# Performance work log

Measured on AMD Instinct MI355X. Metric: run time of the kernel, lower is better.

Reference implementation:

```python
import jax, jax.numpy as jnp
import numpy as np

DIM = 1024
NUM_EXPERTS = 8
TOP_K = 2
HIDDEN = int(DIM * 1.5)  # 1536, matches expert_dim = int(dim * 1.5)


def setup_inputs() -> dict:
    key = jax.random.key(0)
    k_x, k_r, k_w1, k_w2, k_w3 = jax.random.split(key, 5)
    B, T = 2, 4096
    s_in = 1.0 / np.sqrt(DIM)
    s_h = 1.0 / np.sqrt(HIDDEN)
    return {
        "x": jax.random.normal(k_x, (B, T, DIM), dtype=jnp.float32),
        # router: Linear(dim, num_experts, bias=False) -> stored as [C, E]
        "Wr": jax.random.uniform(k_r, (DIM, NUM_EXPERTS), minval=-s_in, maxval=s_in, dtype=jnp.float32),
        # stacked expert weights: w1/w3 [E, C, H], w2 [E, H, C]
        "W1": jax.random.uniform(k_w1, (NUM_EXPERTS, DIM, HIDDEN), minval=-s_in, maxval=s_in, dtype=jnp.float32),
        "W2": jax.random.uniform(k_w2, (NUM_EXPERTS, HIDDEN, DIM), minval=-s_h, maxval=s_h, dtype=jnp.float32),
        "W3": jax.random.uniform(k_w3, (NUM_EXPERTS, DIM, HIDDEN), minval=-s_in, maxval=s_in, dtype=jnp.float32),
    }


def reference(x, Wr, W1, W2, W3):
    B, T, C = x.shape
    xf = x.reshape(-1, C)  # [N, C]
    gate_logits = xf @ Wr  # [N, E]
    w, idx = jax.lax.top_k(gate_logits, TOP_K)  # [N, K]
    w = jax.nn.softmax(w, axis=-1)
    # dense combine weights: zero for non-selected experts -> [N, E]
    comb = jnp.sum(w[:, :, None] * jax.nn.one_hot(idx, NUM_EXPERTS, dtype=w.dtype), axis=1)
    # SwiGLU for all experts (masked-out experts contribute with weight 0)
    h = jnp.einsum('nc,ech->neh', xf, W1)  # [N, E, H]
    g = jnp.einsum('nc,ech->neh', xf, W3)  # [N, E, H]
    y = jnp.einsum('neh,ehc->nec', jax.nn.silu(h) * g, W2)  # [N, E, C]
    out = jnp.einsum('nec,ne->nc', y, comb)
    return out.reshape(B, T, C)
```

## Files before the change

### kernel.cpp

```cpp
#include <hip/hip_runtime.h>
#include <hip/hip_bf16.h>
#include <math.h>

#define DIM   1024
#define NEXP  8
#define HID   1536
#define NTOK  8192
#define NPOS  16384
#define PADR  128

typedef __attribute__((ext_vector_type(8))) short bf16x8;
typedef __attribute__((ext_vector_type(4))) float floatx4;

__device__ __forceinline__ unsigned short f2bf(float f) {
  unsigned int u = __float_as_uint(f);
  u += 0x7FFFu + ((u >> 16) & 1u);
  return (unsigned short)(u >> 16);
}

__device__ __forceinline__ float bf2f(unsigned short h) {
  return __uint_as_float((unsigned int)h << 16);
}

__device__ __forceinline__ void async_cp16(void* lds, const void* g) {
  __builtin_amdgcn_global_load_lds(
      (const __attribute__((address_space(1))) unsigned int*)g,
      (__attribute__((address_space(3))) unsigned int*)lds, 16, 0, 0);
}

__device__ __forceinline__ int2 cnt_off(const int* __restrict__ hdr, int e) {
  int s = 0, c = 0;
#pragma unroll
  for (int i = 0; i < NEXP; ++i) {
    const int v = hdr[i];
    if (i < e) s += v;
    if (i == e) c = v;
  }
  return make_int2(c, s);
}

__global__ __launch_bounds__(256) void moe_router(
    const float* __restrict__ x, const float* __restrict__ Wr,
    int* __restrict__ meta_e, float* __restrict__ meta_w) {
  const int wave = threadIdx.x >> 6, lane = threadIdx.x & 63;
  const int token = blockIdx.x * 4 + wave;
  const float* xr = x + (size_t)token * DIM;
  float acc[NEXP];
#pragma unroll
  for (int e = 0; e < NEXP; ++e) acc[e] = 0.f;
  for (int i = lane; i < DIM; i += 64) {
    const float xv = xr[i];
    const float* wr = Wr + (size_t)i * NEXP;
#pragma unroll
    for (int e = 0; e < NEXP; ++e) acc[e] += xv * wr[e];
  }
#pragma unroll
  for (int off = 32; off > 0; off >>= 1) {
#pragma unroll
    for (int e = 0; e < NEXP; ++e) acc[e] += __shfl_down(acc[e], off);
  }
  if (lane == 0) {
    int i0 = 0; float v0 = acc[0];
#pragma unroll
    for (int e = 1; e < NEXP; ++e) if (acc[e] > v0) { v0 = acc[e]; i0 = e; }
    int i1 = -1; float v1 = -3.4e38f;
#pragma unroll
    for (int e = 0; e < NEXP; ++e) if (e != i0 && acc[e] > v1) { v1 = acc[e]; i1 = e; }
    const float w0 = 1.f / (1.f + expf(v1 - v0));
    meta_e[token * 2 + 0] = i0;
    meta_e[token * 2 + 1] = i1;
    meta_w[token * 2 + 0] = w0;
    meta_w[token * 2 + 1] = 1.f - w0;
  }
}

__global__ __launch_bounds__(256) void moe_hist(
    const int* __restrict__ meta_e, int* __restrict__ hdr) {
  const int idx = blockIdx.x * 256 + threadIdx.x;
  const int lane = threadIdx.x & 63;
  const int e = meta_e[idx];
#pragma unroll
  for (int ex = 0; ex < NEXP; ++ex) {
    const unsigned long long m = __ballot(e == ex);
    if (m && lane == 0) atomicAdd(&hdr[ex], __popcll(m));
  }
}

__global__ __launch_bounds__(256) void moe_build(
    const int* __restrict__ meta_e, int* __restrict__ hdr,
    int* __restrict__ tok, int* __restrict__ inv) {
  const int idx = blockIdx.x * 256 + threadIdx.x;
  const int lane = threadIdx.x & 63;
  const int token = idx >> 1;
  const int e = meta_e[idx];
  int pos = 0;
#pragma unroll
  for (int ex = 0; ex < NEXP; ++ex) {
    const unsigned long long m = __ballot(e == ex);
    if (m) {
      const int leader = (int)__ffsll((long long)m) - 1;
      int base = 0;
      if (lane == leader) base = atomicAdd(&hdr[16 + ex], __popcll(m));
      base = __shfl(base, leader);
      if (e == ex) {
        const int2 co = cnt_off(hdr, ex);
        pos = co.y + base + (int)__popcll(m & ((1ull << lane) - 1ull));
      }
    }
  }
  tok[pos] = token;
  inv[idx] = pos;
}

__global__ __launch_bounds__(256) void moe_gather(
    const float* __restrict__ x, const int* __restrict__ tok,
    unsigned short* __restrict__ Xg) {
  const int pos = blockIdx.x;
  const int t = tok[pos];
  const float4 v = ((const float4*)(x + (size_t)t * DIM))[threadIdx.x];
  ushort4 o = make_ushort4(f2bf(v.x), f2bf(v.y), f2bf(v.z), f2bf(v.w));
  ((ushort4*)(Xg + (size_t)pos * DIM))[threadIdx.x] = o;
}

__global__ __launch_bounds__(256) void moe_transpose_all(
    const float* __restrict__ W1, const float* __restrict__ W3,
    const float* __restrict__ W2,
    unsigned short* __restrict__ W1t, unsigned short* __restrict__ W3t,
    unsigned short* __restrict__ W2t) {
  __shared__ float tile[64][65];
  const int z = blockIdx.z;
  const int which = z >> 3, e = z & 7;
  const float* src; unsigned short* dst; int R, C;
  if (which == 0)      { src = W1; dst = W1t; R = DIM; C = HID; }
  else if (which == 1) { src = W3; dst = W3t; R = DIM; C = HID; }
  else                 { src = W2; dst = W2t; R = HID; C = DIM; }
  const int nbx = C / 64;
  const int bx = blockIdx.x % nbx, by = blockIdx.x / nbx;
  const float* ein = src + (size_t)e * R * C;
  unsigned short* eout = dst + (size_t)e * R * C;
  const int c0 = bx * 64, r0 = by * 64;
  const int lx = threadIdx.x & 15, ly = threadIdx.x >> 4;
#pragma unroll
  for (int it = 0; it < 4; ++it) {
    const int r = ly + it * 16;
    const float4 v = *(const float4*)&ein[(size_t)(r0 + r) * C + c0 + lx * 4];
    tile[r][lx * 4 + 0] = v.x;
    tile[r][lx * 4 + 1] = v.y;
    tile[r][lx * 4 + 2] = v.z;
    tile[r][lx * 4 + 3] = v.w;
  }
  __syncthreads();
#pragma unroll
  for (int it = 0; it < 4; ++it) {
    const int cc = ly + it * 16;
    ushort4 o = make_ushort4(f2bf(tile[lx * 4 + 0][cc]), f2bf(tile[lx * 4 + 1][cc]),
                             f2bf(tile[lx * 4 + 2][cc]), f2bf(tile[lx * 4 + 3][cc]));
    *(ushort4*)&eout[(size_t)(c0 + cc) * R + r0 + lx * 4] = o;
  }
}


__global__ __launch_bounds__(256) void moe_gemm1(
    const unsigned short* __restrict__ Xg,
    const unsigned short* __restrict__ W1t,
    const unsigned short* __restrict__ W3t,
    unsigned short* __restrict__ Hbuf,
    const int* __restrict__ hdr) {
  const int e = blockIdx.y;
  const int NT = HID / 64;
  const int tileRow = blockIdx.x / NT;
  const int tileN = blockIdx.x % NT;
  const int2 co = cnt_off(hdr, e);
  const int cnt = co.x;
  if (tileRow * 128 >= cnt) return;
  const int off = co.y;
  const size_t tileM = (size_t)off + (size_t)tileRow * 128;
  const int n0 = tileN * 64;

  __shared__ unsigned short As[2][128 * 32];
  __shared__ unsigned short B1s[2][64 * 32];
  __shared__ unsigned short B3s[2][64 * 32];

  const int lane = threadIdx.x & 63;
  const int wave = threadIdx.x >> 6;
  const int wm = wave >> 1, wn = wave & 1;
  const int rsub = lane >> 2;
  const int ksw  = (((lane & 3) ^ ((lane >> 3) & 3))) * 8;
  const int kf   = (((lane >> 4) ^ ((lane >> 1) & 3))) * 8;

  const unsigned short* Abase = Xg + tileM * DIM;
  const unsigned short* B1base = W1t + ((size_t)e * HID + n0) * DIM;
  const unsigned short* B3base = W3t + ((size_t)e * HID + n0) * DIM;

  floatx4 zero = {0.f, 0.f, 0.f, 0.f};
  floatx4 acc_h[4][2], acc_g[4][2];
#pragma unroll
  for (int i = 0; i < 4; ++i)
#pragma unroll
    for (int j = 0; j < 2; ++j) { acc_h[i][j] = zero; acc_g[i][j] = zero; }

  for (int k0 = 0; k0 < DIM; k0 += 64) {
#pragma unroll
    for (int h = 0; h < 2; ++h) {
      const int kk = k0 + h * 32;
#pragma unroll
      for (int t = 0; t < 2; ++t) {
        const int c = wave * 2 + t;
        const int row = c * 16 + rsub;
        async_cp16(&As[h][c * 512], Abase + (size_t)row * DIM + kk + ksw);
      }
      const int row = wave * 16 + rsub;
      async_cp16(&B1s[h][wave * 512], B1base + (size_t)row * DIM + kk + ksw);
      async_cp16(&B3s[h][wave * 512], B3base + (size_t)row * DIM + kk + ksw);
    }
    __syncthreads();
#pragma unroll
    for (int h = 0; h < 2; ++h) {
      bf16x8 a[4], b1[2], b3[2];
#pragma unroll
      for (int i = 0; i < 4; ++i)
        a[i] = *(const bf16x8*)&As[h][(wm * 64 + i * 16 + (lane & 15)) * 32 + kf];
#pragma unroll
      for (int j = 0; j < 2; ++j) {
        b1[j] = *(const bf16x8*)&B1s[h][(wn * 32 + j * 16 + (lane & 15)) * 32 + kf];
        b3[j] = *(const bf16x8*)&B3s[h][(wn * 32 + j * 16 + (lane & 15)) * 32 + kf];
      }
#pragma unroll
      for (int i = 0; i < 4; ++i)
#pragma unroll
        for (int j = 0; j < 2; ++j) {
          acc_h[i][j] = __builtin_amdgcn_mfma_f32_16x16x32_bf16(a[i], b1[j], acc_h[i][j], 0, 0, 0);
          acc_g[i][j] = __builtin_amdgcn_mfma_f32_16x16x32_bf16(a[i], b3[j], acc_g[i][j], 0, 0, 0);
        }
    }
    __syncthreads();
  }

  const int r0 = (lane >> 4) * 4;
  const int cc = lane & 15;
#pragma unroll
  for (int i = 0; i < 4; ++i)
#pragma unroll
    for (int r = 0; r < 4; ++r) {
      const int lrow = tileRow * 128 + wm * 64 + i * 16 + r0 + r;
      if (lrow < cnt) {
        unsigned short* hrow = Hbuf + (size_t)(off + lrow) * HID + n0 + wn * 32 + cc;
#pragma unroll
        for (int j = 0; j < 2; ++j) {
          const float h = acc_h[i][j][r];
          const float g = acc_g[i][j][r];
          const float s = h / (1.f + expf(-h));
          hrow[j * 16] = f2bf(s * g);
        }
      }
    }
}

__global__ __launch_bounds__(256) void moe_gemm2(
    const unsigned short* __restrict__ Hbuf,
    const unsigned short* __restrict__ W2t,
    const int* __restrict__ hdr,
    unsigned short* __restrict__ Y) {
  const int e = blockIdx.y;
  const int NT = DIM / 128;
  const int tileRow = blockIdx.x / NT;
  const int tileN = blockIdx.x % NT;
  const int2 co = cnt_off(hdr, e);
  const int cnt = co.x;
  if (tileRow * 128 >= cnt) return;
  const int off = co.y;
  const size_t tileM = (size_t)off + (size_t)tileRow * 128;
  const int n0 = tileN * 128;

  __shared__ unsigned short As[2][128 * 32];
  __shared__ unsigned short Bs[2][128 * 32];

  const int lane = threadIdx.x & 63;
  const int wave = threadIdx.x >> 6;
  const int wm = wave >> 1, wn = wave & 1;
  const int rsub = lane >> 2;
  const int ksw  = (((lane & 3) ^ ((lane >> 3) & 3))) * 8;
  const int kf   = (((lane >> 4) ^ ((lane >> 1) & 3))) * 8;

  const unsigned short* Abase = Hbuf + tileM * HID;
  const unsigned short* Bbase = W2t + ((size_t)e * DIM + n0) * HID;

  floatx4 zero = {0.f, 0.f, 0.f, 0.f};
  floatx4 acc[4][4];
#pragma unroll
  for (int i = 0; i < 4; ++i)
#pragma unroll
    for (int j = 0; j < 4; ++j) acc[i][j] = zero;

  for (int k0 = 0; k0 < HID; k0 += 64) {
#pragma unroll
    for (int h = 0; h < 2; ++h) {
      const int kk = k0 + h * 32;
#pragma unroll
      for (int t = 0; t < 2; ++t) {
        const int c = wave * 2 + t;
        const int row = c * 16 + rsub;
        async_cp16(&As[h][c * 512], Abase + (size_t)row * HID + kk + ksw);
      }
#pragma unroll
      for (int t = 0; t < 2; ++t) {
        const int c = wave * 2 + t;
        const int row = c * 16 + rsub;
        async_cp16(&Bs[h][c * 512], Bbase + (size_t)row * HID + kk + ksw);
      }
    }
    __syncthreads();
#pragma unroll
    for (int h = 0; h < 2; ++h) {
      bf16x8 a[4], b[4];
#pragma unroll
      for (int i = 0; i < 4; ++i)
        a[i] = *(const bf16x8*)&As[h][(wm * 64 + i * 16 + (lane & 15)) * 32 + kf];
#pragma unroll
      for (int j = 0; j < 4; ++j)
        b[j] = *(const bf16x8*)&Bs[h][(wn * 64 + j * 16 + (lane & 15)) * 32 + kf];
#pragma unroll
      for (int i = 0; i < 4; ++i)
#pragma unroll
        for (int j = 0; j < 4; ++j)
          acc[i][j] = __builtin_amdgcn_mfma_f32_16x16x32_bf16(a[i], b[j], acc[i][j], 0, 0, 0);
    }
    __syncthreads();
  }

  const int r0 = (lane >> 4) * 4;
  const int cc = lane & 15;
#pragma unroll
  for (int i = 0; i < 4; ++i)
#pragma unroll
    for (int r = 0; r < 4; ++r) {
      const int lrow = tileRow * 128 + wm * 64 + i * 16 + r0 + r;
      if (lrow < cnt) {
        unsigned short* yrow = Y + (size_t)(off + lrow) * DIM + n0 + wn * 64 + cc;
#pragma unroll
        for (int j = 0; j < 4; ++j)
          yrow[j * 16] = f2bf(acc[i][j][r]);
      }
    }
}

__global__ __launch_bounds__(256) void moe_combine(
    const unsigned short* __restrict__ Y, const int* __restrict__ inv,
    const float* __restrict__ meta_w, float* __restrict__ out) {
  const int t = blockIdx.x;
  const int p0 = inv[t * 2 + 0], p1 = inv[t * 2 + 1];
  const float w0 = meta_w[t * 2 + 0], w1 = meta_w[t * 2 + 1];
  const ushort4 a = ((const ushort4*)(Y + (size_t)p0 * DIM))[threadIdx.x];
  const ushort4 b = ((const ushort4*)(Y + (size_t)p1 * DIM))[threadIdx.x];
  float4 o;
  o.x = w0 * bf2f(a.x) + w1 * bf2f(b.x);
  o.y = w0 * bf2f(a.y) + w1 * bf2f(b.y);
  o.z = w0 * bf2f(a.z) + w1 * bf2f(b.z);
  o.w = w0 * bf2f(a.w) + w1 * bf2f(b.w);
  ((float4*)(out + (size_t)t * DIM))[threadIdx.x] = o;
}

extern "C" void kernel_launch(void* const* d_in, const int* in_sizes, int n_in,
                              void* d_out, int out_size, void* d_ws, size_t ws_size,
                              hipStream_t stream) {
  const float* x  = (const float*)d_in[0];
  const float* Wr = (const float*)d_in[1];
  const float* W1 = (const float*)d_in[2];
  const float* W2 = (const float*)d_in[3];
  const float* W3 = (const float*)d_in[4];
  float* out = (float*)d_out;

  char* p = (char*)d_ws;
  auto carve = [&](size_t bytes) { char* r = p; p += (bytes + 255) & ~(size_t)255; return r; };

  int*            hdr    = (int*)carve(256);
  int*            meta_e = (int*)carve((size_t)NTOK * 2 * sizeof(int));
  float*          meta_w = (float*)carve((size_t)NTOK * 2 * sizeof(float));
  int*            tok    = (int*)carve((size_t)NPOS * sizeof(int));
  int*            inv    = (int*)carve((size_t)NTOK * 2 * sizeof(int));
  unsigned short* Xg     = (unsigned short*)carve((size_t)(NPOS + PADR) * DIM * 2);
  unsigned short* Hbuf   = (unsigned short*)carve((size_t)(NPOS + PADR) * HID * 2);
  unsigned short* W1t    = (unsigned short*)carve((size_t)NEXP * HID * DIM * 2);
  unsigned short* W3t    = (unsigned short*)carve((size_t)NEXP * HID * DIM * 2);
  unsigned short* W2t    = (unsigned short*)carve((size_t)NEXP * DIM * HID * 2);
  unsigned short* Y      = Xg;

  hipMemsetAsync(hdr, 0, 256, stream);

  moe_router<<<NTOK / 4, 256, 0, stream>>>(x, Wr, meta_e, meta_w);
  moe_hist<<<NPOS / 256, 256, 0, stream>>>(meta_e, hdr);
  moe_build<<<NPOS / 256, 256, 0, stream>>>(meta_e, hdr, tok, inv);
  moe_gather<<<NPOS, 256, 0, stream>>>(x, tok, Xg);

  moe_transpose_all<<<dim3(384, 1, 24), dim3(256), 0, stream>>>(W1, W3, W2, W1t, W3t, W2t);

  moe_gemm1<<<dim3(64 * (HID / 64), NEXP), 256, 0, stream>>>(Xg, W1t, W3t, Hbuf, hdr);
  moe_gemm2<<<dim3(64 * (DIM / 128), NEXP), 256, 0, stream>>>(Hbuf, W2t, hdr, Y);
  moe_combine<<<NTOK, 256, 0, stream>>>(Y, inv, meta_w, out);
}
```

Before: 525.8 us.

## Double-buffer MoE GEMM K-loop, persistent tile-row loop, wider transpose stores

Both expert GEMMs now issue async copies for the next 32-wide K slice into the alternate LDS buffer while computing on the current one, replacing the load-all-then-compute pattern with one sync per slice. The grid is shrunk so each block loops over tile rows with stride 16 instead of launching 64 row slots and exiting early, which cuts idle block launches. The weight transpose now writes 16-byte packed bf16 stores instead of 8-byte ones. The risk is less parallelism per expert when token counts are unbalanced, and extra LDS reads in the transpose may cause bank conflicts.

```diff
diff --git a/kernel.cpp b/kernel.cpp
--- a/kernel.cpp
+++ b/kernel.cpp
@@ -150,12 +150,17 @@
     tile[r][lx * 4 + 3] = v.w;
   }
   __syncthreads();
-#pragma unroll
-  for (int it = 0; it < 4; ++it) {
-    const int cc = ly + it * 16;
-    ushort4 o = make_ushort4(f2bf(tile[lx * 4 + 0][cc]), f2bf(tile[lx * 4 + 1][cc]),
-                             f2bf(tile[lx * 4 + 2][cc]), f2bf(tile[lx * 4 + 3][cc]));
-    *(ushort4*)&eout[(size_t)(c0 + cc) * R + r0 + lx * 4] = o;
+  const int r8 = (threadIdx.x & 7) * 8;
+  const int ccb = threadIdx.x >> 3;
+#pragma unroll
+  for (int it = 0; it < 2; ++it) {
+    const int cc = ccb + it * 32;
+    unsigned int w0 = (unsigned int)f2bf(tile[r8 + 0][cc]) | ((unsigned int)f2bf(tile[r8 + 1][cc]) << 16);
+    unsigned int w1 = (unsigned int)f2bf(tile[r8 + 2][cc]) | ((unsigned int)f2bf(tile[r8 + 3][cc]) << 16);
+    unsigned int w2 = (unsigned int)f2bf(tile[r8 + 4][cc]) | ((unsigned int)f2bf(tile[r8 + 5][cc]) << 16);
+    unsigned int w3 = (unsigned int)f2bf(tile[r8 + 6][cc]) | ((unsigned int)f2bf(tile[r8 + 7][cc]) << 16);
+    uint4 o = make_uint4(w0, w1, w2, w3);
+    *(uint4*)&eout[(size_t)(c0 + cc) * R + r0 + r8] = o;
   }
 }
 
@@ -168,13 +173,12 @@
     const int* __restrict__ hdr) {
   const int e = blockIdx.y;
   const int NT = HID / 64;
-  const int tileRow = blockIdx.x / NT;
+  const int TROW = 16;
   const int tileN = blockIdx.x % NT;
+  const int tr0 = blockIdx.x / NT;
   const int2 co = cnt_off(hdr, e);
   const int cnt = co.x;
-  if (tileRow * 128 >= cnt) return;
   const int off = co.y;
-  const size_t tileM = (size_t)off + (size_t)tileRow * 128;
   const int n0 = tileN * 64;
 
   __shared__ unsigned short As[2][128 * 32];
@@ -188,72 +192,77 @@
   const int ksw  = (((lane & 3) ^ ((lane >> 3) & 3))) * 8;
   const int kf   = (((lane >> 4) ^ ((lane >> 1) & 3))) * 8;
 
-  const unsigned short* Abase = Xg + tileM * DIM;
   const unsigned short* B1base = W1t + ((size_t)e * HID + n0) * DIM;
   const unsigned short* B3base = W3t + ((size_t)e * HID + n0) * DIM;
+  const unsigned short* Abase;
 
   floatx4 zero = {0.f, 0.f, 0.f, 0.f};
   floatx4 acc_h[4][2], acc_g[4][2];
-#pragma unroll
-  for (int i = 0; i < 4; ++i)
-#pragma unroll
-    for (int j = 0; j < 2; ++j) { acc_h[i][j] = zero; acc_g[i][j] = zero; }
-
-  for (int k0 = 0; k0 < DIM; k0 += 64) {
-#pragma unroll
-    for (int h = 0; h < 2; ++h) {
-      const int kk = k0 + h * 32;
-#pragma unroll
-      for (int t = 0; t < 2; ++t) {
-        const int c = wave * 2 + t;
-        const int row = c * 16 + rsub;
-        async_cp16(&As[h][c * 512], Abase + (size_t)row * DIM + kk + ksw);
+
+  auto stage = [&](int b, int kk) {
+#pragma unroll
+    for (int t2 = 0; t2 < 2; ++t2) {
+      const int c = wave * 2 + t2;
+      async_cp16(&As[b][c * 512], Abase + (size_t)(c * 16 + rsub) * DIM + kk + ksw);
+    }
+    async_cp16(&B1s[b][wave * 512], B1base + (size_t)(wave * 16 + rsub) * DIM + kk + ksw);
+    async_cp16(&B3s[b][wave * 512], B3base + (size_t)(wave * 16 + rsub) * DIM + kk + ksw);
+  };
+  auto compute = [&](int b) {
+    bf16x8 a[4], b1[2], b3[2];
+#pragma unroll
+    for (int i = 0; i < 4; ++i)
+      a[i] = *(const bf16x8*)&As[b][(wm * 64 + i * 16 + (lane & 15)) * 32 + kf];
+#pragma unroll
+    for (int j = 0; j < 2; ++j) {
+      b1[j] = *(const bf16x8*)&B1s[b][(wn * 32 + j * 16 + (lane & 15)) * 32 + kf];
+      b3[j] = *(const bf16x8*)&B3s[b][(wn * 32 + j * 16 + (lane & 15)) * 32 + kf];
+    }
+#pragma unroll
+    for (int i = 0; i < 4; ++i)
+#pragma unroll
+      for (int j = 0; j < 2; ++j) {
+        acc_h[i][j] = __builtin_amdgcn_mfma_f32_16x16x32_bf16(a[i], b1[j], acc_h[i][j], 0, 0, 0);
+        acc_g[i][j] = __builtin_amdgcn_mfma_f32_16x16x32_bf16(a[i], b3[j], acc_g[i][j], 0, 0, 0);
       }
-      const int row = wave * 16 + rsub;
-      async_cp16(&B1s[h][wave * 512], B1base + (size_t)row * DIM + kk + ksw);
-      async_cp16(&B3s[h][wave * 512], B3base + (size_t)row * DIM + kk + ksw);
-    }
+  };
+
+  for (int tileRow = tr0; tileRow * 128 < cnt; tileRow += TROW) {
+    Abase = Xg + ((size_t)off + (size_t)tileRow * 128) * DIM;
+#pragma unroll
+    for (int i = 0; i < 4; ++i)
+#pragma unroll
+      for (int j = 0; j < 2; ++j) { acc_h[i][j] = zero; acc_g[i][j] = zero; }
+
+    stage(0, 0);
     __syncthreads();
-#pragma unroll
-    for (int h = 0; h < 2; ++h) {
-      bf16x8 a[4], b1[2], b3[2];
-#pragma unroll
-      for (int i = 0; i < 4; ++i)
-        a[i] = *(const bf16x8*)&As[h][(wm * 64 + i * 16 + (lane & 15)) * 32 + kf];
-#pragma unroll
-      for (int j = 0; j < 2; ++j) {
-        b1[j] = *(const bf16x8*)&B1s[h][(wn * 32 + j * 16 + (lane & 15)) * 32 + kf];
-        b3[j] = *(const bf16x8*)&B3s[h][(wn * 32 + j * 16 + (lane & 15)) * 32 + kf];
-      }
-#pragma unroll
-      for (int i = 0; i < 4; ++i)
-#pragma unroll
-        for (int j = 0; j < 2; ++j) {
-          acc_h[i][j] = __builtin_amdgcn_mfma_f32_16x16x32_bf16(a[i], b1[j], acc_h[i][j], 0, 0, 0);
-          acc_g[i][j] = __builtin_amdgcn_mfma_f32_16x16x32_bf16(a[i], b3[j], acc_g[i][j], 0, 0, 0);
-        }
-    }
-    __syncthreads();
-  }
-
-  const int r0 = (lane >> 4) * 4;
-  const int cc = lane & 15;
-#pragma unroll
-  for (int i = 0; i < 4; ++i)
-#pragma unroll
-    for (int r = 0; r < 4; ++r) {
-      const int lrow = tileRow * 128 + wm * 64 + i * 16 + r0 + r;
-      if (lrow < cnt) {
-        unsigned short* hrow = Hbuf + (size_t)(off + lrow) * HID + n0 + wn * 32 + cc;
-#pragma unroll
-        for (int j = 0; j < 2; ++j) {
-          const float h = acc_h[i][j][r];
-          const float g = acc_g[i][j][r];
-          const float s = h / (1.f + expf(-h));
-          hrow[j * 16] = f2bf(s * g);
+#pragma unroll 1
+    for (int kt = 0; kt < 15; ++kt) {
+      stage(1, (2 * kt + 1) * 32); compute(0); __syncthreads();
+      stage(0, (2 * kt + 2) * 32); compute(1); __syncthreads();
+    }
+    stage(1, 31 * 32); compute(0); __syncthreads();
+    compute(1);
+
+    const int r0 = (lane >> 4) * 4;
+    const int cc = lane & 15;
+#pragma unroll
+    for (int i = 0; i < 4; ++i)
+#pragma unroll
+      for (int r = 0; r < 4; ++r) {
+        const int lrow = tileRow * 128 + wm * 64 + i * 16 + r0 + r;
+        if (lrow < cnt) {
+          unsigned short* hrow = Hbuf + (size_t)(off + lrow) * HID + n0 + wn * 32 + cc;
+#pragma unroll
+          for (int j = 0; j < 2; ++j) {
+            const float h = acc_h[i][j][r];
+            const float g = acc_g[i][j][r];
+            const float s = h / (1.f + expf(-h));
+            hrow[j * 16] = f2bf(s * g);
+          }
         }
       }
-    }
+  }
 }
 
 __global__ __launch_bounds__(256) void moe_gemm2(
@@ -263,13 +272,12 @@
     unsigned short* __restrict__ Y) {
   const int e = blockIdx.y;
   const int NT = DIM / 128;
-  const int tileRow = blockIdx.x / NT;
+  const int TROW = 16;
   const int tileN = blockIdx.x % NT;
+  const int tr0 = blockIdx.x / NT;
   const int2 co = cnt_off(hdr, e);
   const int cnt = co.x;
-  if (tileRow * 128 >= cnt) return;
   const int off = co.y;
-  const size_t tileM = (size_t)off + (size_t)tileRow * 128;
   const int n0 = tileN * 128;
 
   __shared__ unsigned short As[2][128 * 32];
@@ -282,66 +290,67 @@
   const int ksw  = (((lane & 3) ^ ((lane >> 3) & 3))) * 8;
   const int kf   = (((lane >> 4) ^ ((lane >> 1) & 3))) * 8;
 
-  const unsigned short* Abase = Hbuf + tileM * HID;
   const unsigned short* Bbase = W2t + ((size_t)e * DIM + n0) * HID;
+  const unsigned short* Abase;
 
   floatx4 zero = {0.f, 0.f, 0.f, 0.f};
   floatx4 acc[4][4];
-#pragma unroll
-  for (int i = 0; i < 4; ++i)
-#pragma unroll
-    for (int j = 0; j < 4; ++j) acc[i][j] = zero;
-
-  for (int k0 = 0; k0 < HID; k0 += 64) {
-#pragma unroll
-    for (int h = 0; h < 2; ++h) {
-      const int kk = k0 + h * 32;
-#pragma unroll
-      for (int t = 0; t < 2; ++t) {
-        const int c = wave * 2 + t;
-        const int row = c * 16 + rsub;
-        async_cp16(&As[h][c * 512], Abase + (size_t)row * HID + kk + ksw);
+
+  auto stage = [&](int b, int kk) {
+#pragma unroll
+    for (int t2 = 0; t2 < 2; ++t2) {
+      const int c = wave * 2 + t2;
+      async_cp16(&As[b][c * 512], Abase + (size_t)(c * 16 + rsub) * HID + kk + ksw);
+      async_cp16(&Bs[b][c * 512], Bbase + (size_t)(c * 16 + rsub) * HID + kk + ksw);
+    }
+  };
+  auto compute = [&](int bb) {
+    bf16x8 a[4], b[4];
+#pragma unroll
+    for (int i = 0; i < 4; ++i)
+      a[i] = *(const bf16x8*)&As[bb][(wm * 64 + i * 16 + (lane & 15)) * 32 + kf];
+#pragma unroll
+    for (int j = 0; j < 4; ++j)
+      b[j] = *(const bf16x8*)&Bs[bb][(wn * 64 + j * 16 + (lane & 15)) * 32 + kf];
+#pragma unroll
+    for (int i = 0; i < 4; ++i)
+#pragma unroll
+      for (int j = 0; j < 4; ++j)
+        acc[i][j] = __builtin_amdgcn_mfma_f32_16x16x32_bf16(a[i], b[j], acc[i][j], 0, 0, 0);
+  };
+
+  for (int tileRow = tr0; tileRow * 128 < cnt; tileRow += TROW) {
+    Abase = Hbuf + ((size_t)off + (size_t)tileRow * 128) * HID;
+#pragma unroll
+    for (int i = 0; i < 4; ++i)
+#pragma unroll
+      for (int j = 0; j < 4; ++j) acc[i][j] = zero;
+
+    stage(0, 0);
+    __syncthreads();
+#pragma unroll 1
+    for (int kt = 0; kt < 23; ++kt) {
+      stage(1, (2 * kt + 1) * 32); compute(0); __syncthreads();
+      stage(0, (2 * kt + 2) * 32); compute(1); __syncthreads();
+    }
+    stage(1, 47 * 32); compute(0); __syncthreads();
+    compute(1);
+
+    const int r0 = (lane >> 4) * 4;
+    const int cc = lane & 15;
+#pragma unroll
+    for (int i = 0; i < 4; ++i)
+#pragma unroll
+      for (int r = 0; r < 4; ++r) {
+        const int lrow = tileRow * 128 + wm * 64 + i * 16 + r0 + r;
+        if (lrow < cnt) {
+          unsigned short* yrow = Y + (size_t)(off + lrow) * DIM + n0 + wn * 64 + cc;
+#pragma unroll
+          for (int j = 0; j < 4; ++j)
+            yrow[j * 16] = f2bf(acc[i][j][r]);
+        }
       }
-#pragma unroll
-      for (int t = 0; t < 2; ++t) {
-        const int c = wave * 2 + t;
-        const int row = c * 16 + rsub;
-        async_cp16(&Bs[h][c * 512], Bbase + (size_t)row * HID + kk + ksw);
-      }
-    }
-    __syncthreads();
-#pragma unroll
-    for (int h = 0; h < 2; ++h) {
-      bf16x8 a[4], b[4];
-#pragma unroll
-      for (int i = 0; i < 4; ++i)
-        a[i] = *(const bf16x8*)&As[h][(wm * 64 + i * 16 + (lane & 15)) * 32 + kf];
-#pragma unroll
-      for (int j = 0; j < 4; ++j)
-        b[j] = *(const bf16x8*)&Bs[h][(wn * 64 + j * 16 + (lane & 15)) * 32 + kf];
-#pragma unroll
-      for (int i = 0; i < 4; ++i)
-#pragma unroll
-        for (int j = 0; j < 4; ++j)
-          acc[i][j] = __builtin_amdgcn_mfma_f32_16x16x32_bf16(a[i], b[j], acc[i][j], 0, 0, 0);
-    }
-    __syncthreads();
-  }
-
-  const int r0 = (lane >> 4) * 4;
-  const int cc = lane & 15;
-#pragma unroll
-  for (int i = 0; i < 4; ++i)
-#pragma unroll
-    for (int r = 0; r < 4; ++r) {
-      const int lrow = tileRow * 128 + wm * 64 + i * 16 + r0 + r;
-      if (lrow < cnt) {
-        unsigned short* yrow = Y + (size_t)(off + lrow) * DIM + n0 + wn * 64 + cc;
-#pragma unroll
-        for (int j = 0; j < 4; ++j)
-          yrow[j * 16] = f2bf(acc[i][j][r]);
-      }
-    }
+  }
 }
 
 __global__ __launch_bounds__(256) void moe_combine(
@@ -394,7 +403,7 @@
 
   moe_transpose_all<<<dim3(384, 1, 24), dim3(256), 0, stream>>>(W1, W3, W2, W1t, W3t, W2t);
 
-  moe_gemm1<<<dim3(64 * (HID / 64), NEXP), 256, 0, stream>>>(Xg, W1t, W3t, Hbuf, hdr);
-  moe_gemm2<<<dim3(64 * (DIM / 128), NEXP), 256, 0, stream>>>(Hbuf, W2t, hdr, Y);
+  moe_gemm1<<<dim3(16 * (HID / 64), NEXP), 256, 0, stream>>>(Xg, W1t, W3t, Hbuf, hdr);
+  moe_gemm2<<<dim3(16 * (DIM / 128), NEXP), 256, 0, stream>>>(Hbuf, W2t, hdr, Y);
   moe_combine<<<NTOK, 256, 0, stream>>>(Y, inv, meta_w, out);
 }
```

Measured after the change: 622.6 us. +18.4%, slower.

## Fuse router, histogram and weight transpose; scatter-add combine into down-proj epilogue

Applied to the files above, without the earlier changes.

Merges the router, the expert histogram (now counted in LDS per block) and the weight transpose/bf16 conversion into one launch, and the transpose now writes 16-byte packed stores. It removes the separate combine kernel: gemm2 scales each row by its routing weight and atomically adds fp32 results straight into the output, which is zero-filled by a memset. This saves launches and the bf16 Y round trip, but adds fp32 atomics on the output and makes the summation order nondeterministic.

```diff
diff --git a/kernel.cpp b/kernel.cpp
--- a/kernel.cpp
+++ b/kernel.cpp
@@ -39,56 +39,100 @@
   return make_int2(c, s);
 }
 
-__global__ __launch_bounds__(256) void moe_router(
+__global__ __launch_bounds__(256) void moe_router_transpose(
     const float* __restrict__ x, const float* __restrict__ Wr,
-    int* __restrict__ meta_e, float* __restrict__ meta_w) {
-  const int wave = threadIdx.x >> 6, lane = threadIdx.x & 63;
-  const int token = blockIdx.x * 4 + wave;
-  const float* xr = x + (size_t)token * DIM;
-  float acc[NEXP];
-#pragma unroll
-  for (int e = 0; e < NEXP; ++e) acc[e] = 0.f;
-  for (int i = lane; i < DIM; i += 64) {
-    const float xv = xr[i];
-    const float* wr = Wr + (size_t)i * NEXP;
-#pragma unroll
-    for (int e = 0; e < NEXP; ++e) acc[e] += xv * wr[e];
-  }
-#pragma unroll
-  for (int off = 32; off > 0; off >>= 1) {
-#pragma unroll
-    for (int e = 0; e < NEXP; ++e) acc[e] += __shfl_down(acc[e], off);
-  }
-  if (lane == 0) {
-    int i0 = 0; float v0 = acc[0];
-#pragma unroll
-    for (int e = 1; e < NEXP; ++e) if (acc[e] > v0) { v0 = acc[e]; i0 = e; }
-    int i1 = -1; float v1 = -3.4e38f;
-#pragma unroll
-    for (int e = 0; e < NEXP; ++e) if (e != i0 && acc[e] > v1) { v1 = acc[e]; i1 = e; }
-    const float w0 = 1.f / (1.f + expf(v1 - v0));
-    meta_e[token * 2 + 0] = i0;
-    meta_e[token * 2 + 1] = i1;
-    meta_w[token * 2 + 0] = w0;
-    meta_w[token * 2 + 1] = 1.f - w0;
-  }
-}
-
-__global__ __launch_bounds__(256) void moe_hist(
-    const int* __restrict__ meta_e, int* __restrict__ hdr) {
-  const int idx = blockIdx.x * 256 + threadIdx.x;
-  const int lane = threadIdx.x & 63;
-  const int e = meta_e[idx];
-#pragma unroll
-  for (int ex = 0; ex < NEXP; ++ex) {
-    const unsigned long long m = __ballot(e == ex);
-    if (m && lane == 0) atomicAdd(&hdr[ex], __popcll(m));
+    int* __restrict__ meta_e, float* __restrict__ meta_w,
+    int* __restrict__ hdr,
+    const float* __restrict__ W1, const float* __restrict__ W3,
+    const float* __restrict__ W2,
+    unsigned short* __restrict__ W1t, unsigned short* __restrict__ W3t,
+    unsigned short* __restrict__ W2t) {
+  __shared__ float tile[64][65];
+  __shared__ int hcnt[8];
+
+  if (blockIdx.x < (NTOK / 4)) {
+    if (threadIdx.x < 8) hcnt[threadIdx.x] = 0;
+    __syncthreads();
+    const int wave = threadIdx.x >> 6, lane = threadIdx.x & 63;
+    const int token = blockIdx.x * 4 + wave;
+    const float* xr = x + (size_t)token * DIM;
+    float acc[NEXP];
+#pragma unroll
+    for (int e = 0; e < NEXP; ++e) acc[e] = 0.f;
+    for (int i = lane; i < DIM; i += 64) {
+      const float xv = xr[i];
+      const float* wr = Wr + (size_t)i * NEXP;
+#pragma unroll
+      for (int e = 0; e < NEXP; ++e) acc[e] += xv * wr[e];
+    }
+#pragma unroll
+    for (int off = 32; off > 0; off >>= 1) {
+#pragma unroll
+      for (int e = 0; e < NEXP; ++e) acc[e] += __shfl_down(acc[e], off);
+    }
+    if (lane == 0) {
+      int i0 = 0; float v0 = acc[0];
+#pragma unroll
+      for (int e = 1; e < NEXP; ++e) if (acc[e] > v0) { v0 = acc[e]; i0 = e; }
+      int i1 = -1; float v1 = -3.4e38f;
+#pragma unroll
+      for (int e = 0; e < NEXP; ++e) if (e != i0 && acc[e] > v1) { v1 = acc[e]; i1 = e; }
+      const float w0 = 1.f / (1.f + expf(v1 - v0));
+      meta_e[token * 2 + 0] = i0;
+      meta_e[token * 2 + 1] = i1;
+      meta_w[token * 2 + 0] = w0;
+      meta_w[token * 2 + 1] = 1.f - w0;
+      atomicAdd(&hcnt[i0], 1);
+      atomicAdd(&hcnt[i1], 1);
+    }
+    __syncthreads();
+    if (threadIdx.x < 8) {
+      const int c = hcnt[threadIdx.x];
+      if (c) atomicAdd(&hdr[threadIdx.x], c);
+    }
+    return;
+  }
+
+  const int id = blockIdx.x - (NTOK / 4);
+  const int tz = id / 384, tx = id % 384;
+  const int which = tz >> 3, e = tz & 7;
+  const float* src; unsigned short* dst; int R, C;
+  if (which == 0)      { src = W1; dst = W1t; R = DIM; C = HID; }
+  else if (which == 1) { src = W3; dst = W3t; R = DIM; C = HID; }
+  else                 { src = W2; dst = W2t; R = HID; C = DIM; }
+  const int nbx = C / 64;
+  const int bx = tx % nbx, by = tx / nbx;
+  const float* ein = src + (size_t)e * R * C;
+  unsigned short* eout = dst + (size_t)e * R * C;
+  const int c0 = bx * 64, r0 = by * 64;
+  const int lx = threadIdx.x & 15, ly = threadIdx.x >> 4;
+#pragma unroll
+  for (int it = 0; it < 4; ++it) {
+    const int r = ly + it * 16;
+    const float4 v = *(const float4*)&ein[(size_t)(r0 + r) * C + c0 + lx * 4];
+    tile[r][lx * 4 + 0] = v.x;
+    tile[r][lx * 4 + 1] = v.y;
+    tile[r][lx * 4 + 2] = v.z;
+    tile[r][lx * 4 + 3] = v.w;
+  }
+  __syncthreads();
+  const int r8 = (threadIdx.x & 7) * 8;
+  const int ccb = threadIdx.x >> 3;
+#pragma unroll
+  for (int it = 0; it < 2; ++it) {
+    const int cc = ccb + it * 32;
+    unsigned int w0 = (unsigned int)f2bf(tile[r8 + 0][cc]) | ((unsigned int)f2bf(tile[r8 + 1][cc]) << 16);
+    unsigned int w1 = (unsigned int)f2bf(tile[r8 + 2][cc]) | ((unsigned int)f2bf(tile[r8 + 3][cc]) << 16);
+    unsigned int w2 = (unsigned int)f2bf(tile[r8 + 4][cc]) | ((unsigned int)f2bf(tile[r8 + 5][cc]) << 16);
+    unsigned int w3 = (unsigned int)f2bf(tile[r8 + 6][cc]) | ((unsigned int)f2bf(tile[r8 + 7][cc]) << 16);
+    uint4 o = make_uint4(w0, w1, w2, w3);
+    *(uint4*)&eout[(size_t)(c0 + cc) * R + r0 + r8] = o;
   }
 }
 
 __global__ __launch_bounds__(256) void moe_build(
-    const int* __restrict__ meta_e, int* __restrict__ hdr,
-    int* __restrict__ tok, int* __restrict__ inv) {
+    const int* __restrict__ meta_e, const float* __restrict__ meta_w,
+    int* __restrict__ hdr, int* __restrict__ tok, float* __restrict__ wpos) {
   const int idx = blockIdx.x * 256 + threadIdx.x;
   const int lane = threadIdx.x & 63;
   const int token = idx >> 1;
@@ -109,7 +153,7 @@
     }
   }
   tok[pos] = token;
-  inv[idx] = pos;
+  wpos[pos] = meta_w[idx];
 }
 
 __global__ __launch_bounds__(256) void moe_gather(
@@ -120,43 +164,6 @@
   const float4 v = ((const float4*)(x + (size_t)t * DIM))[threadIdx.x];
   ushort4 o = make_ushort4(f2bf(v.x), f2bf(v.y), f2bf(v.z), f2bf(v.w));
   ((ushort4*)(Xg + (size_t)pos * DIM))[threadIdx.x] = o;
-}
-
-__global__ __launch_bounds__(256) void moe_transpose_all(
-    const float* __restrict__ W1, const float* __restrict__ W3,
-    const float* __restrict__ W2,
-    unsigned short* __restrict__ W1t, unsigned short* __restrict__ W3t,
-    unsigned short* __restrict__ W2t) {
-  __shared__ float tile[64][65];
-  const int z = blockIdx.z;
-  const int which = z >> 3, e = z & 7;
-  const float* src; unsigned short* dst; int R, C;
-  if (which == 0)      { src = W1; dst = W1t; R = DIM; C = HID; }
-  else if (which == 1) { src = W3; dst = W3t; R = DIM; C = HID; }
-  else                 { src = W2; dst = W2t; R = HID; C = DIM; }
-  const int nbx = C / 64;
-  const int bx = blockIdx.x % nbx, by = blockIdx.x / nbx;
-  const float* ein = src + (size_t)e * R * C;
-  unsigned short* eout = dst + (size_t)e * R * C;
-  const int c0 = bx * 64, r0 = by * 64;
-  const int lx = threadIdx.x & 15, ly = threadIdx.x >> 4;
-#pragma unroll
-  for (int it = 0; it < 4; ++it) {
-    const int r = ly + it * 16;
-    const float4 v = *(const float4*)&ein[(size_t)(r0 + r) * C + c0 + lx * 4];
-    tile[r][lx * 4 + 0] = v.x;
-    tile[r][lx * 4 + 1] = v.y;
-    tile[r][lx * 4 + 2] = v.z;
-    tile[r][lx * 4 + 3] = v.w;
-  }
-  __syncthreads();
-#pragma unroll
-  for (int it = 0; it < 4; ++it) {
-    const int cc = ly + it * 16;
-    ushort4 o = make_ushort4(f2bf(tile[lx * 4 + 0][cc]), f2bf(tile[lx * 4 + 1][cc]),
-                             f2bf(tile[lx * 4 + 2][cc]), f2bf(tile[lx * 4 + 3][cc]));
-    *(ushort4*)&eout[(size_t)(c0 + cc) * R + r0 + lx * 4] = o;
-  }
 }
 
 
@@ -260,7 +267,8 @@
     const unsigned short* __restrict__ Hbuf,
     const unsigned short* __restrict__ W2t,
     const int* __restrict__ hdr,
-    unsigned short* __restrict__ Y) {
+    const int* __restrict__ tok, const float* __restrict__ wpos,
+    float* __restrict__ out) {
   const int e = blockIdx.y;
   const int NT = DIM / 128;
   const int tileRow = blockIdx.x / NT;
@@ -336,28 +344,15 @@
     for (int r = 0; r < 4; ++r) {
       const int lrow = tileRow * 128 + wm * 64 + i * 16 + r0 + r;
       if (lrow < cnt) {
-        unsigned short* yrow = Y + (size_t)(off + lrow) * DIM + n0 + wn * 64 + cc;
+        const int pos = off + lrow;
+        const int t = tok[pos];
+        const float w = wpos[pos];
+        float* orow = out + (size_t)t * DIM + n0 + wn * 64 + cc;
 #pragma unroll
         for (int j = 0; j < 4; ++j)
-          yrow[j * 16] = f2bf(acc[i][j][r]);
-      }
-    }
-}
-
-__global__ __launch_bounds__(256) void moe_combine(
-    const unsigned short* __restrict__ Y, const int* __restrict__ inv,
-    const float* __restrict__ meta_w, float* __restrict__ out) {
-  const int t = blockIdx.x;
-  const int p0 = inv[t * 2 + 0], p1 = inv[t * 2 + 1];
-  const float w0 = meta_w[t * 2 + 0], w1 = meta_w[t * 2 + 1];
-  const ushort4 a = ((const ushort4*)(Y + (size_t)p0 * DIM))[threadIdx.x];
-  const ushort4 b = ((const ushort4*)(Y + (size_t)p1 * DIM))[threadIdx.x];
-  float4 o;
-  o.x = w0 * bf2f(a.x) + w1 * bf2f(b.x);
-  o.y = w0 * bf2f(a.y) + w1 * bf2f(b.y);
-  o.z = w0 * bf2f(a.z) + w1 * bf2f(b.z);
-  o.w = w0 * bf2f(a.w) + w1 * bf2f(b.w);
-  ((float4*)(out + (size_t)t * DIM))[threadIdx.x] = o;
+          atomicAdd(&orow[j * 16], w * acc[i][j][r]);
+      }
+    }
 }
 
 extern "C" void kernel_launch(void* const* d_in, const int* in_sizes, int n_in,
@@ -377,24 +372,21 @@
   int*            meta_e = (int*)carve((size_t)NTOK * 2 * sizeof(int));
   float*          meta_w = (float*)carve((size_t)NTOK * 2 * sizeof(float));
   int*            tok    = (int*)carve((size_t)NPOS * sizeof(int));
-  int*            inv    = (int*)carve((size_t)NTOK * 2 * sizeof(int));
+  float*          wpos   = (float*)carve((size_t)NPOS * sizeof(float));
   unsigned short* Xg     = (unsigned short*)carve((size_t)(NPOS + PADR) * DIM * 2);
   unsigned short* Hbuf   = (unsigned short*)carve((size_t)(NPOS + PADR) * HID * 2);
   unsigned short* W1t    = (unsigned short*)carve((size_t)NEXP * HID * DIM * 2);
   unsigned short* W3t    = (unsigned short*)carve((size_t)NEXP * HID * DIM * 2);
   unsigned short* W2t    = (unsigned short*)carve((size_t)NEXP * DIM * HID * 2);
-  unsigned short* Y      = Xg;
 
   hipMemsetAsync(hdr, 0, 256, stream);
-
-  moe_router<<<NTOK / 4, 256, 0, stream>>>(x, Wr, meta_e, meta_w);
-  moe_hist<<<NPOS / 256, 256, 0, stream>>>(meta_e, hdr);
-  moe_build<<<NPOS / 256, 256, 0, stream>>>(meta_e, hdr, tok, inv);
+  hipMemsetAsync(out, 0, (size_t)NTOK * DIM * sizeof(float), stream);
+
+  moe_router_transpose<<<NTOK / 4 + 24 * 384, 256, 0, stream>>>(
+      x, Wr, meta_e, meta_w, hdr, W1, W3, W2, W1t, W3t, W2t);
+  moe_build<<<NPOS / 256, 256, 0, stream>>>(meta_e, meta_w, hdr, tok, wpos);
   moe_gather<<<NPOS, 256, 0, stream>>>(x, tok, Xg);
 
-  moe_transpose_all<<<dim3(384, 1, 24), dim3(256), 0, stream>>>(W1, W3, W2, W1t, W3t, W2t);
-
   moe_gemm1<<<dim3(64 * (HID / 64), NEXP), 256, 0, stream>>>(Xg, W1t, W3t, Hbuf, hdr);
-  moe_gemm2<<<dim3(64 * (DIM / 128), NEXP), 256, 0, stream>>>(Hbuf, W2t, hdr, Y);
-  moe_combine<<<NTOK, 256, 0, stream>>>(Y, inv, meta_w, out);
-}
+  moe_gemm2<<<dim3(64 * (DIM / 128), NEXP), 256, 0, stream>>>(Hbuf, W2t, hdr, tok, wpos, out);
+}
```

Result: no change. 519.1 us (-1.3%).
